# Kernel tuning notes

Hardware: AMD Instinct MI355X
Metric: run time of the kernel (lower is better)

The kernel has to match this reference:

```python
import jax, jax.numpy as jnp
import numpy as np

B = 100000      # query points
L = 8           # num levels
N_RBF = 256     # RBF centers per level
F = 16          # features per level
OUT = 3         # output dim


def setup_inputs() -> dict:
    key = jax.random.key(0)
    k = jax.random.split(key, 6)
    x = jax.random.normal(k[0], (B, 3), dtype=jnp.float32)
    # small-magnitude features so gaussian RBF responses are non-degenerate
    feats = 0.1 * jax.random.normal(k[1], (B, L * F), dtype=jnp.float32)
    # centers initialized uniform(-1e-4, 1e-4) as in the torch module
    centers = jax.random.uniform(k[2], (L, N_RBF, F), dtype=jnp.float32,
                                 minval=-1e-4, maxval=1e-4)
    # log-width parameters (exp'd in forward); small perturbation around 0
    betas = 0.01 * jax.random.normal(k[3], (L, N_RBF, F), dtype=jnp.float32)
    W = jax.random.normal(k[4], (OUT, N_RBF * L), dtype=jnp.float32) / np.sqrt(N_RBF * L)
    b = jax.random.normal(k[5], (OUT,), dtype=jnp.float32) * 0.01
    return {"x": x, "feats": feats, "centers": centers, "betas": betas, "W": W, "b": b}


def reference(x, feats, centers, betas, W, b):
    # centers, betas: [L, N, F]. x is unused by the original forward (faithful).
    Lnum, N, f = centers.shape
    rbfs = []
    for i in range(Lnum):
        # concat of first i+1 per-level tables along feature axis -> [N, (i+1)*f]
        C = centers[: i + 1].transpose(1, 0, 2).reshape(N, (i + 1) * f)
        Bw = jnp.exp(betas[: i + 1].transpose(1, 0, 2).reshape(N, (i + 1) * f))
        x_in = feats[:, : (i + 1) * f]                      # [B, (i+1)*f]
        term1 = (x_in * x_in) @ Bw.T                        # [B, N]
        term2 = x_in @ (Bw * C).T                           # [B, N]
        term3 = jnp.sum(Bw * C * C, axis=1)                 # [N]
        dist_sq = term1 - 2.0 * term2 + term3[None, :]
        rbfs.append(jnp.exp(-0.5 * dist_sq))                # gaussian basis
    outs = jnp.concatenate(rbfs, axis=-1)                   # [B, L*N]
    return outs @ W.T + b
```

## Files before the change

kernel.cpp:

```cpp
#include <hip/hip_runtime.h>
#include <math.h>

#define LN 8
#define NRBF 256
#define FD 16
#define OUTD 3
#define KC (-0.72134752044f)

typedef __attribute__((ext_vector_type(8))) short short8;
typedef __attribute__((ext_vector_type(4))) float floatx4;
typedef __attribute__((ext_vector_type(2))) float floatx2;

__device__ __forceinline__ short f2bf(float f) {
    unsigned u = __builtin_bit_cast(unsigned, f);
    u += 0x7fffu + ((u >> 16) & 1u);
    return (short)(u >> 16);
}


__global__ __launch_bounds__(256) void prep(
    const float* __restrict__ centers, const float* __restrict__ betas,
    const float* __restrict__ W, short* __restrict__ PKB, float* __restrict__ EPI)
{
    __shared__ float ls[LN * 32];
    int blk = blockIdx.x;
    int tid = threadIdx.x;
    if (blk < 32) {
        int g    = blk * 256 + tid;
        int lane = g & 63;
        int j    = (g >> 6) & 7;
        int nt   = g >> 9;
        int n    = nt * 16 + (lane & 15);
        int kq   = lane >> 4;
        size_t base = ((size_t)(j * NRBF + n)) * FD + kq * 4;
        float4 bq = *(const float4*)(betas + base);
        float4 cq = *(const float4*)(centers + base);
        float a0 = KC * __expf(bq.x), a1 = KC * __expf(bq.y);
        float a2 = KC * __expf(bq.z), a3 = KC * __expf(bq.w);
        short8 v;
        v[0] = f2bf(a0); v[1] = f2bf(-2.0f * a0 * cq.x);
        v[2] = f2bf(a1); v[3] = f2bf(-2.0f * a1 * cq.y);
        v[4] = f2bf(a2); v[5] = f2bf(-2.0f * a2 * cq.z);
        v[6] = f2bf(a3); v[7] = f2bf(-2.0f * a3 * cq.w);
        *((short8*)(PKB + (size_t)g * 8)) = v;
    } else {
        int jj = tid >> 5;
        int nl = tid & 31;
        int n  = (blk - 32) * 32 + nl;
        const float* bp = betas   + ((size_t)(jj * NRBF + n)) * FD;
        const float* cp = centers + ((size_t)(jj * NRBF + n)) * FD;
        float s = 0.f;
#pragma unroll
        for (int q = 0; q < 4; ++q) {
            float4 bq = *(const float4*)(bp + q * 4);
            float4 cq = *(const float4*)(cp + q * 4);
            s = fmaf(__expf(bq.x) * cq.x, cq.x, s);
            s = fmaf(__expf(bq.y) * cq.y, cq.y, s);
            s = fmaf(__expf(bq.z) * cq.z, cq.z, s);
            s = fmaf(__expf(bq.w) * cq.w, cq.w, s);
        }
        ls[jj * 32 + nl] = s;
        __syncthreads();
        float t3 = 0.f;
        for (int j2 = 0; j2 <= jj; ++j2) t3 += ls[j2 * 32 + nl];
        float E = __builtin_amdgcn_exp2f(KC * t3);
        float4 e;
        e.x = W[0 * (LN * NRBF) + jj * NRBF + n] * E;
        e.y = W[1 * (LN * NRBF) + jj * NRBF + n] * E;
        e.z = W[2 * (LN * NRBF) + jj * NRBF + n] * E;
        e.w = 0.f;
        ((float4*)EPI)[((size_t)(n >> 4) * 128) + jj * 16 + (n & 15)] = e;
    }
}

#define CVT(dst, vv)  do {                                         \
        short8 f_;                                                 \
        f_[0] = f2bf((vv).x * (vv).x); f_[1] = f2bf((vv).x);       \
        f_[2] = f2bf((vv).y * (vv).y); f_[3] = f2bf((vv).y);       \
        f_[4] = f2bf((vv).z * (vv).z); f_[5] = f2bf((vv).z);       \
        f_[6] = f2bf((vv).w * (vv).w); f_[7] = f2bf((vv).w);       \
        (dst) = f_; } while (0)

__global__ __launch_bounds__(256) void rbf_mfma(
    const float* __restrict__ feats, const short* __restrict__ PKB,
    const float* __restrict__ EPI, const float* __restrict__ bias,
    float* __restrict__ out, int B)
{
    __shared__ short8 pk_s[2][8 * 64];
    __shared__ float4 ep_s[2][8 * 16];

    int tid  = threadIdx.x;
    int lane = tid & 63;
    int w    = tid >> 6;
    int ntile = (B + 31) >> 5;
    int tile = blockIdx.x * 4 + w;
    bool tvalid = (tile < ntile);
    if (!tvalid) tile = ntile - 1;
    int b0 = tile * 32;
    int m  = lane & 15;
    int kq = lane >> 4;
    int brow0 = b0 + m;      if (brow0 >= B) brow0 = B - 1;
    int brow1 = b0 + 16 + m; if (brow1 >= B) brow1 = B - 1;
    const float* xrow0 = feats + (size_t)brow0 * (LN * FD) + kq * 4;
    const float* xrow1 = feats + (size_t)brow1 * (LN * FD) + kq * 4;

#define STAGE(buf, ntv)                                                         \
    do {                                                                        \
        _Pragma("unroll")                                                       \
        for (int q = 0; q < 2; ++q) {                                           \
            const short* gp = PKB + ((size_t)(ntv) * 512 + w * 128 + q * 64 + lane) * 8; \
            __builtin_amdgcn_global_load_lds(                                   \
                (const __attribute__((address_space(1))) void*)gp,              \
                (__attribute__((address_space(3))) void*)&pk_s[buf][w * 128 + q * 64], \
                16, 0, 0);                                                      \
        }                                                                       \
        if (lane < 32) {                                                        \
            const float* ge = EPI + ((size_t)(ntv) * 128 + w * 32 + lane) * 4;  \
            __builtin_amdgcn_global_load_lds(                                   \
                (const __attribute__((address_space(1))) void*)ge,              \
                (__attribute__((address_space(3))) void*)&ep_s[buf][w * 32],    \
                16, 0, 0);                                                      \
        }                                                                       \
    } while (0)

#define EXPPROJ(accv, ev, oo, zz)                                  \
    do {                                                           \
        floatx2 exy_ = { (ev).x, (ev).y };                         \
        floatx2 ezz_ = { (ev).z, (ev).z };                         \
        float rv0_ = __builtin_amdgcn_exp2f((accv)[0]);            \
        float rv1_ = __builtin_amdgcn_exp2f((accv)[1]);            \
        float rv2_ = __builtin_amdgcn_exp2f((accv)[2]);            \
        float rv3_ = __builtin_amdgcn_exp2f((accv)[3]);            \
        oo[0] += (floatx2){rv0_, rv0_} * exy_;                     \
        oo[1] += (floatx2){rv1_, rv1_} * exy_;                     \
        oo[2] += (floatx2){rv2_, rv2_} * exy_;                     \
        oo[3] += (floatx2){rv3_, rv3_} * exy_;                     \
        zz[0] += (floatx2){rv0_, rv1_} * ezz_;                     \
        zz[1] += (floatx2){rv2_, rv3_} * ezz_;                     \
    } while (0)

    STAGE(0, 0);

    short8 af0[LN], af1[LN];
#pragma unroll
    for (int j = 0; j < LN; ++j) {
        float4 xa = *(const float4*)(xrow0 + j * FD);
        float4 xb = *(const float4*)(xrow1 + j * FD);
        CVT(af0[j], xa);
        CVT(af1[j], xb);
    }

    floatx2 o01A[4], o01B[4];
    floatx2 ozA[2],  ozB[2];
#pragma unroll
    for (int r = 0; r < 4; ++r) { o01A[r] = (floatx2){0.f, 0.f}; o01B[r] = (floatx2){0.f, 0.f}; }
    ozA[0] = (floatx2){0.f, 0.f}; ozA[1] = (floatx2){0.f, 0.f};
    ozB[0] = (floatx2){0.f, 0.f}; ozB[1] = (floatx2){0.f, 0.f};

    __syncthreads();

#pragma unroll 1
    for (int nt = 0; nt < 16; ++nt) {
        int cur = nt & 1;
        if (nt < 15) STAGE(cur ^ 1, nt + 1);

        floatx4 accA = (floatx4){0.f, 0.f, 0.f, 0.f};
        floatx4 accB = (floatx4){0.f, 0.f, 0.f, 0.f};
        floatx4 accpA, accpB;

#pragma unroll
        for (int j = 0; j < LN; ++j) {
            short8 bf = pk_s[cur][j * 64 + lane];
            accA = __builtin_amdgcn_mfma_f32_16x16x32_bf16(af0[j], bf, accA, 0, 0, 0);
            accB = __builtin_amdgcn_mfma_f32_16x16x32_bf16(af1[j], bf, accB, 0, 0, 0);
            if (j > 0) {
                float4 e = ep_s[cur][(j - 1) * 16 + m];
                EXPPROJ(accpA, e, o01A, ozA);
                EXPPROJ(accpB, e, o01B, ozB);
            }
            accpA = accA;
            accpB = accB;
        }
        {
            float4 e = ep_s[cur][7 * 16 + m];
            EXPPROJ(accpA, e, o01A, ozA);
            EXPPROJ(accpB, e, o01B, ozB);
        }
        __syncthreads();
    }
#undef STAGE
#undef EXPPROJ

    float oacc[24];
#pragma unroll
    for (int r = 0; r < 4; ++r) {
        oacc[r * 3 + 0]  = o01A[r].x;
        oacc[r * 3 + 1]  = o01A[r].y;
        oacc[r * 3 + 2]  = (r & 1) ? ozA[r >> 1].y : ozA[r >> 1].x;
        oacc[12 + r * 3 + 0] = o01B[r].x;
        oacc[12 + r * 3 + 1] = o01B[r].y;
        oacc[12 + r * 3 + 2] = (r & 1) ? ozB[r >> 1].y : ozB[r >> 1].x;
    }
#pragma unroll
    for (int i = 0; i < 24; ++i) {
        oacc[i] += __shfl_xor(oacc[i], 1);
        oacc[i] += __shfl_xor(oacc[i], 2);
        oacc[i] += __shfl_xor(oacc[i], 4);
        oacc[i] += __shfl_xor(oacc[i], 8);
    }

    if (tvalid && m < OUTD) {
        float bv = bias[m];
#pragma unroll
        for (int r = 0; r < 4; ++r) {
            int row0 = b0 + kq * 4 + r;
            int row1 = b0 + 16 + kq * 4 + r;
            if (row0 < B) out[(size_t)row0 * OUTD + m] = oacc[r * 3 + m] + bv;
            if (row1 < B) out[(size_t)row1 * OUTD + m] = oacc[12 + r * 3 + m] + bv;
        }
    }
}

extern "C" void kernel_launch(void* const* d_in, const int* in_sizes, int n_in,
                              void* d_out, int out_size, void* d_ws, size_t ws_size,
                              hipStream_t stream) {
    const float* feats   = (const float*)d_in[1];
    const float* centers = (const float*)d_in[2];
    const float* betas   = (const float*)d_in[3];
    const float* W       = (const float*)d_in[4];
    const float* bias    = (const float*)d_in[5];
    float* out = (float*)d_out;
    int B = in_sizes[1] / (LN * FD);

    short* PKB = (short*)d_ws;
    float* EPI = (float*)((char*)d_ws + 65536 * 2);

    prep<<<40, 256, 0, stream>>>(centers, betas, W, PKB, EPI);

    int tiles  = (B + 31) / 32;
    int blocks = (tiles + 3) / 4;
    rbf_mfma<<<blocks, 256, 0, stream>>>(feats, PKB, EPI, bias, out, B);
}
```

Measured before the change: 157.5 us.

## Replace LDS staging with per-wave register prefetch of packed B operands

Removes the shared-memory double buffer and block-wide barriers. Each wave now loads its packed B fragments and epilogue coefficients straight from global memory (L2/L1-cached) into registers, using a software prefetch ring about four steps ahead. Blocks shrink to one wave, so there is one tile per block and no __syncthreads. The trade-off is more redundant global/L1 traffic per wave and higher register pressure in exchange for dropping LDS round-trips and synchronization.

```diff
diff --git a/kernel.cpp b/kernel.cpp
--- a/kernel.cpp
+++ b/kernel.cpp
@@ -81,19 +81,14 @@
         f_[6] = f2bf((vv).w * (vv).w); f_[7] = f2bf((vv).w);       \
         (dst) = f_; } while (0)
 
-__global__ __launch_bounds__(256) void rbf_mfma(
+__global__ __launch_bounds__(64) void rbf_mfma(
     const float* __restrict__ feats, const short* __restrict__ PKB,
     const float* __restrict__ EPI, const float* __restrict__ bias,
     float* __restrict__ out, int B)
 {
-    __shared__ short8 pk_s[2][8 * 64];
-    __shared__ float4 ep_s[2][8 * 16];
-
-    int tid  = threadIdx.x;
-    int lane = tid & 63;
-    int w    = tid >> 6;
+    int lane = threadIdx.x & 63;
     int ntile = (B + 31) >> 5;
-    int tile = blockIdx.x * 4 + w;
+    int tile = blockIdx.x;
     bool tvalid = (tile < ntile);
     if (!tvalid) tile = ntile - 1;
     int b0 = tile * 32;
@@ -104,24 +99,10 @@
     const float* xrow0 = feats + (size_t)brow0 * (LN * FD) + kq * 4;
     const float* xrow1 = feats + (size_t)brow1 * (LN * FD) + kq * 4;
 
-#define STAGE(buf, ntv)                                                         \
-    do {                                                                        \
-        _Pragma("unroll")                                                       \
-        for (int q = 0; q < 2; ++q) {                                           \
-            const short* gp = PKB + ((size_t)(ntv) * 512 + w * 128 + q * 64 + lane) * 8; \
-            __builtin_amdgcn_global_load_lds(                                   \
-                (const __attribute__((address_space(1))) void*)gp,              \
-                (__attribute__((address_space(3))) void*)&pk_s[buf][w * 128 + q * 64], \
-                16, 0, 0);                                                      \
-        }                                                                       \
-        if (lane < 32) {                                                        \
-            const float* ge = EPI + ((size_t)(ntv) * 128 + w * 32 + lane) * 4;  \
-            __builtin_amdgcn_global_load_lds(                                   \
-                (const __attribute__((address_space(1))) void*)ge,              \
-                (__attribute__((address_space(3))) void*)&ep_s[buf][w * 32],    \
-                16, 0, 0);                                                      \
-        }                                                                       \
-    } while (0)
+    const short8* pkb8 = (const short8*)PKB;
+    const float4* epi4 = (const float4*)EPI;
+    const short8* pb = pkb8 + lane;
+    const float4* eb = epi4 + m;
 
 #define EXPPROJ(accv, ev, oo, zz)                                  \
     do {                                                           \
@@ -139,8 +120,6 @@
         zz[1] += (floatx2){rv2_, rv3_} * ezz_;                     \
     } while (0)
 
-    STAGE(0, 0);
-
     short8 af0[LN], af1[LN];
 #pragma unroll
     for (int j = 0; j < LN; ++j) {
@@ -157,38 +136,52 @@
     ozA[0] = (floatx2){0.f, 0.f}; ozA[1] = (floatx2){0.f, 0.f};
     ozB[0] = (floatx2){0.f, 0.f}; ozB[1] = (floatx2){0.f, 0.f};
 
-    __syncthreads();
+    short8 bf0 = pb[0 * 64], bf1 = pb[1 * 64], bf2 = pb[2 * 64], bf3 = pb[3 * 64];
+    float4 ep0 = eb[0 * 16], ep1 = eb[1 * 16], ep2 = eb[2 * 16], ep3 = eb[3 * 16];
+
+    floatx4 accA, accB, accpA, accpB;
+
+#define MSTEP(J, BF, BNEXT, EP, ENEXT)                                       \
+    do {                                                                     \
+        accA = __builtin_amdgcn_mfma_f32_16x16x32_bf16(af0[J], BF, accA, 0, 0, 0); \
+        accB = __builtin_amdgcn_mfma_f32_16x16x32_bf16(af1[J], BF, accB, 0, 0, 0); \
+        BF = BNEXT;                                                          \
+        { float4 e_ = EP; EP = ENEXT;                                        \
+          EXPPROJ(accpA, e_, o01A, ozA);                                     \
+          EXPPROJ(accpB, e_, o01B, ozB); }                                   \
+        accpA = accA; accpB = accB;                                          \
+    } while (0)
 
 #pragma unroll 1
     for (int nt = 0; nt < 16; ++nt) {
-        int cur = nt & 1;
-        if (nt < 15) STAGE(cur ^ 1, nt + 1);
-
-        floatx4 accA = (floatx4){0.f, 0.f, 0.f, 0.f};
-        floatx4 accB = (floatx4){0.f, 0.f, 0.f, 0.f};
-        floatx4 accpA, accpB;
-
-#pragma unroll
-        for (int j = 0; j < LN; ++j) {
-            short8 bf = pk_s[cur][j * 64 + lane];
-            accA = __builtin_amdgcn_mfma_f32_16x16x32_bf16(af0[j], bf, accA, 0, 0, 0);
-            accB = __builtin_amdgcn_mfma_f32_16x16x32_bf16(af1[j], bf, accB, 0, 0, 0);
-            if (j > 0) {
-                float4 e = ep_s[cur][(j - 1) * 16 + m];
-                EXPPROJ(accpA, e, o01A, ozA);
-                EXPPROJ(accpB, e, o01B, ozB);
-            }
-            accpA = accA;
-            accpB = accB;
+        const short8* pc = pb + (size_t)nt * 512;
+        const float4* ec = eb + (size_t)nt * 128;
+        const short8* pn = (nt < 15) ? (pc + 512) : pc;
+        const float4* en = (nt < 15) ? (ec + 128) : ec;
+
+        accA = (floatx4){0.f, 0.f, 0.f, 0.f};
+        accB = (floatx4){0.f, 0.f, 0.f, 0.f};
+
+        accA = __builtin_amdgcn_mfma_f32_16x16x32_bf16(af0[0], bf0, accA, 0, 0, 0);
+        accB = __builtin_amdgcn_mfma_f32_16x16x32_bf16(af1[0], bf0, accB, 0, 0, 0);
+        bf0 = pc[4 * 64];
+        accpA = accA; accpB = accB;
+
+        MSTEP(1, bf1, pc[5 * 64], ep0, ec[4 * 16]);
+        MSTEP(2, bf2, pc[6 * 64], ep1, ec[5 * 16]);
+        MSTEP(3, bf3, pc[7 * 64], ep2, ec[6 * 16]);
+        MSTEP(4, bf0, pn[0 * 64], ep3, ec[7 * 16]);
+        MSTEP(5, bf1, pn[1 * 64], ep0, en[0 * 16]);
+        MSTEP(6, bf2, pn[2 * 64], ep1, en[1 * 16]);
+        MSTEP(7, bf3, pn[3 * 64], ep2, en[2 * 16]);
+
+        {
+            float4 e_ = ep3; ep3 = en[3 * 16];
+            EXPPROJ(accpA, e_, o01A, ozA);
+            EXPPROJ(accpB, e_, o01B, ozB);
         }
-        {
-            float4 e = ep_s[cur][7 * 16 + m];
-            EXPPROJ(accpA, e, o01A, ozA);
-            EXPPROJ(accpB, e, o01B, ozB);
-        }
-        __syncthreads();
-    }
-#undef STAGE
+    }
+#undef MSTEP
 #undef EXPPROJ
 
     float oacc[24];
@@ -237,7 +230,6 @@
 
     prep<<<40, 256, 0, stream>>>(centers, betas, W, PKB, EPI);
 
-    int tiles  = (B + 31) / 32;
-    int blocks = (tiles + 3) / 4;
-    rbf_mfma<<<blocks, 256, 0, stream>>>(feats, PKB, EPI, bias, out, B);
-}
+    int tiles = (B + 31) / 32;
+    rbf_mfma<<<tiles, 64, 0, stream>>>(feats, PKB, EPI, bias, out, B);
+}
```

New measurement: 147.4 us. -6.4%, faster.
